# Kernel tuning notes

Measured on AMD Instinct MI355X. Metric: run time of the kernel, lower is better.

## Reference

```python
import jax, jax.numpy as jnp
import numpy as np

N_NODES = 100000
N_EDGES = 1600000
K = 48

def setup_inputs() -> dict:
    key = jax.random.key(0)
    ks = jax.random.split(key, 6)
    x = jax.random.normal(ks[0], (N_NODES, K), dtype=jnp.float32)
    pos_edge_index = jax.random.randint(ks[1], (2, N_EDGES), 0, N_NODES, dtype=jnp.int64)
    neg_edge_index = jax.random.randint(ks[2], (2, N_EDGES), 0, N_NODES, dtype=jnp.int64)
    # nn.Linear-style init (uniform +-1/sqrt(fan_in))
    lim1 = 1.0 / np.sqrt(3 * K)
    W1 = jax.random.uniform(ks[3], (3 * K, 16), minval=-lim1, maxval=lim1, dtype=jnp.float32)
    b1 = jnp.zeros((16,), dtype=jnp.float32)
    lim2 = 1.0 / np.sqrt(16)
    W2 = jax.random.uniform(ks[4], (16, K), minval=-lim2, maxval=lim2, dtype=jnp.float32)
    b2 = jnp.zeros((K,), dtype=jnp.float32)
    return {"x": x, "pos_edge_index": pos_edge_index, "neg_edge_index": neg_edge_index,
            "W1": W1, "b1": b1, "W2": W2, "b2": b2}

def _scatter_add_mp(x, edge_index):
    # PyG MessagePassing(aggr='add'), message = x_j:
    # gather source-node features and scatter-add into target nodes.
    src, dst = edge_index[0], edge_index[1]
    msgs = x[src]  # [E, k]
    return jax.ops.segment_sum(msgs, dst, num_segments=x.shape[0])  # [N, k]

def reference(x, pos_edge_index, neg_edge_index, W1, b1, W2, b2):
    x_pos = _scatter_add_mp(x, pos_edge_index)
    x_neg = _scatter_add_mp(x, neg_edge_index)
    out_cat = jnp.concatenate([x, x_pos, x_neg], axis=1)  # [N, 3k]
    h = jnp.tanh(out_cat @ W1 + b1)                        # [N, 16]
    C = h @ W2 + b2                                        # [N, k]
    return jax.nn.softmax(C, axis=1)
```

## Files before the change

### kernel.cpp

```cpp
#include <hip/hip_runtime.h>
#include <hip/hip_fp16.h>
#include <math.h>

#define NN 100000
#define NE 1600000
#define KF 48
#define NEDGE_ALL (2 * NE)

#define BKT_NODES 128
#define NBKT_PER  782
#define NBKT      1564
#define PACK_EPB  4096
#define NPB       782
#define OT2       1566
#define CAP2      2432
#define KSTG      10

typedef _Float16 half2v __attribute__((ext_vector_type(2)));
typedef _Float16 half4v __attribute__((ext_vector_type(4)));

#if defined(__has_builtin)
#if __has_builtin(__builtin_amdgcn_fdot2)
#define HAVE_FDOT2 1
#endif
#endif

__device__ __forceinline__ void acc_pair(float& ax, float& ay, half2v v)
{
#ifdef HAVE_FDOT2
    ax = __builtin_amdgcn_fdot2(v, (half2v){(_Float16)1.f, (_Float16)0.f}, ax, false);
    ay = __builtin_amdgcn_fdot2(v, (half2v){(_Float16)0.f, (_Float16)1.f}, ay, false);
#else
    ax += (float)v.x;
    ay += (float)v.y;
#endif
}

__global__ __launch_bounds__(512) void pack_kernel(
    const float* __restrict__ x,
    const int* __restrict__ ei_pos,
    const int* __restrict__ ei_neg,
    unsigned short* __restrict__ offT,
    unsigned* __restrict__ plist,
    __half* __restrict__ xh)
{
    {
        const float2* __restrict__ x2 = (const float2*)x;
        half2v* __restrict__ xhw = (half2v*)xh;
        const int n2 = (NN + 2) * (KF / 2);
        for (int i = blockIdx.x * 512 + threadIdx.x; i < n2; i += NPB * 512) {
            float2 v = (i < NN * (KF / 2)) ? x2[i] : make_float2(0.f, 0.f);
            xhw[i] = (half2v){(_Float16)v.x, (_Float16)v.y};
        }
    }

    __shared__ int cnt[NBKT];
    __shared__ int ps[391];
    __shared__ unsigned stage[PACK_EPB];

    const int t = threadIdx.x;
    for (int i = t; i < NBKT; i += 512) cnt[i] = 0;
    __syncthreads();

    unsigned pk[8];
    int bk[8];
    const int blockBase = blockIdx.x * PACK_EPB;
#pragma unroll
    for (int j = 0; j < 8; ++j) {
        int e = blockBase + j * 512 + t;
        bk[j] = -1;
        if (e < NEDGE_ALL) {
            int list = e >= NE;
            int ee = list ? e - NE : e;
            const int* ei = list ? ei_neg : ei_pos;
            int src = ei[ee];
            int dst = ei[NE + ee];
            int b = list * NBKT_PER + (dst >> 7);
            bk[j] = b;
            pk[j] = ((unsigned)(dst & 127) << 17) | (unsigned)src;
            atomicAdd(&cnt[b], 1);
        }
    }
    __syncthreads();

    int s0 = 0, s1 = 0, s2 = 0, s3 = 0;
    if (t < 391) {
        s0 = cnt[4 * t]; s1 = cnt[4 * t + 1]; s2 = cnt[4 * t + 2]; s3 = cnt[4 * t + 3];
        ps[t] = s0 + s1 + s2 + s3;
    }
    __syncthreads();
    for (int d = 1; d < 391; d <<= 1) {
        int v = (t < 391 && t >= d) ? ps[t - d] : 0;
        __syncthreads();
        if (t < 391) ps[t] += v;
        __syncthreads();
    }
    unsigned short* myrow = offT + (long)blockIdx.x * OT2;
    if (t < 391) {
        int base = t ? ps[t - 1] : 0;
        int o0 = base, o1 = o0 + s0, o2 = o1 + s1, o3 = o2 + s2;
        myrow[4 * t]     = (unsigned short)o0;
        myrow[4 * t + 1] = (unsigned short)o1;
        myrow[4 * t + 2] = (unsigned short)o2;
        myrow[4 * t + 3] = (unsigned short)o3;
        cnt[4 * t] = o0; cnt[4 * t + 1] = o1; cnt[4 * t + 2] = o2; cnt[4 * t + 3] = o3;
    }
    if (t == 390) myrow[NBKT] = (unsigned short)ps[390];
    __syncthreads();

#pragma unroll
    for (int j = 0; j < 8; ++j) {
        if (bk[j] >= 0) {
            int slot = atomicAdd(&cnt[bk[j]], 1);
            stage[slot] = pk[j];
        }
    }
    __syncthreads();

    {
        const uint4* __restrict__ st4 = (const uint4*)stage;
        uint4* __restrict__ out4 = (uint4*)(plist + (long)blockIdx.x * PACK_EPB);
#pragma unroll
        for (int j = 0; j < 2; ++j)
            out4[j * 512 + t] = st4[j * 512 + t];
    }
}

__global__ __launch_bounds__(256) void gather_kernel(
    const __half* __restrict__ xh,
    const unsigned* __restrict__ plist,
    const unsigned short* __restrict__ offT,
    float* __restrict__ xpos,
    float* __restrict__ xneg)
{
    __shared__ unsigned srt[CAP2];
    __shared__ int rb[NPB + 2];
    __shared__ unsigned short rsL[NPB];
    __shared__ int tmp[196];
    __shared__ int nh[BKT_NODES];
    __shared__ int starts[BKT_NODES];
    __shared__ int ends[BKT_NODES];
    __shared__ int cur2[BKT_NODES];

    const int b = blockIdx.x;
    const int t = threadIdx.x;

    for (int r = t; r < NPB; r += 256) {
        int s = offT[(long)r * OT2 + b];
        int e = offT[(long)r * OT2 + b + 1];
        rsL[r] = (unsigned short)s;
        srt[r] = (unsigned)(e - s);
    }
    if (t < BKT_NODES) nh[t] = 0;
    __syncthreads();

    int s0 = 0, s1 = 0, s2 = 0, s3 = 0;
    if (t < 196) {
        int i0 = 4 * t;
        s0 = (i0     < NPB) ? (int)srt[i0]     : 0;
        s1 = (i0 + 1 < NPB) ? (int)srt[i0 + 1] : 0;
        s2 = (i0 + 2 < NPB) ? (int)srt[i0 + 2] : 0;
        s3 = (i0 + 3 < NPB) ? (int)srt[i0 + 3] : 0;
        tmp[t] = s0 + s1 + s2 + s3;
    }
    __syncthreads();
    for (int d = 1; d < 196; d <<= 1) {
        int v = (t < 196 && t >= d) ? tmp[t - d] : 0;
        __syncthreads();
        if (t < 196) tmp[t] += v;
        __syncthreads();
    }
    if (t < 196) {
        int base = t ? tmp[t - 1] : 0;
        int i0 = 4 * t;
        if (i0     <= NPB) rb[i0]     = base;
        if (i0 + 1 <= NPB) rb[i0 + 1] = base + s0;
        if (i0 + 2 <= NPB) rb[i0 + 2] = base + s0 + s1;
        if (i0 + 3 <= NPB) rb[i0 + 3] = base + s0 + s1 + s2;
    }
    __syncthreads();
    int cb = rb[NPB];
    if (cb > CAP2) cb = CAP2;

    unsigned held[KSTG];
#pragma unroll
    for (int k = 0; k < KSTG; ++k) {
        int i = t + k * 256;
        held[k] = 0;
        if (i < cb) {
            int lo = 0, hi = NPB - 1;
#pragma unroll
            for (int it = 0; it < 10; ++it) {
                int mid = (lo + hi + 1) >> 1;
                bool ge = (rb[mid] <= i);
                lo = ge ? mid : lo;
                hi = ge ? hi : mid - 1;
            }
            unsigned p = plist[(long)lo * PACK_EPB + rsL[lo] + (i - rb[lo])];
            held[k] = p;
            atomicAdd(&nh[p >> 17], 1);
        }
    }
    __syncthreads();

    for (int d = 1; d < BKT_NODES; d <<= 1) {
        int v = 0;
        if (t < BKT_NODES && t >= d) v = nh[t - d];
        __syncthreads();
        if (t < BKT_NODES) nh[t] += v;
        __syncthreads();
    }
    if (t < BKT_NODES) {
        int e_ = min(nh[t], CAP2);
        int s_ = t ? min(nh[t - 1], CAP2) : 0;
        starts[t] = s_;
        ends[t] = e_;
        cur2[t] = s_;
    }
    __syncthreads();

#pragma unroll
    for (int k = 0; k < KSTG; ++k) {
        int i = t + k * 256;
        if (i < cb) {
            unsigned p = held[k];
            int slot = atomicAdd(&cur2[p >> 17], 1);
            if (slot < CAP2) srt[slot] = p;
        }
    }
    __syncthreads();

    const int wave = t >> 6, lane = t & 63;
    const int g = lane >> 4;
    const int sub = lane & 15;
    const int subc = (sub < 12) ? sub : 11;
    const int list = b >= NBKT_PER;
    const int nb = list ? b - NBKT_PER : b;
    float* o = list ? xneg : xpos;
    const half4v* __restrict__ xh4 = (const half4v*)xh;

    for (int n = wave; n < BKT_NODES; n += 4) {
        int gn = nb * BKT_NODES + n;
        if (gn >= NN) continue;
        int s = starts[n], e = ends[n];
        float a0 = 0.f, a1 = 0.f, a2 = 0.f, a3 = 0.f;
        for (int j = s; j < e; j += 16) {
            int i0 = j + g, i1 = j + 4 + g, i2 = j + 8 + g, i3 = j + 12 + g;
            int q0 = (i0 < e) ? (int)(srt[i0 < CAP2 ? i0 : 0] & 0x1FFFFu) : NN;
            int q1 = (i1 < e) ? (int)(srt[i1 < CAP2 ? i1 : 0] & 0x1FFFFu) : NN;
            int q2 = (i2 < e) ? (int)(srt[i2 < CAP2 ? i2 : 0] & 0x1FFFFu) : NN;
            int q3 = (i3 < e) ? (int)(srt[i3 < CAP2 ? i3 : 0] & 0x1FFFFu) : NN;
            half4v v0 = xh4[q0 * 12 + subc];
            half4v v1 = xh4[q1 * 12 + subc];
            half4v v2 = xh4[q2 * 12 + subc];
            half4v v3 = xh4[q3 * 12 + subc];
            acc_pair(a0, a1, (half2v){v0.x, v0.y});
            acc_pair(a2, a3, (half2v){v0.z, v0.w});
            acc_pair(a0, a1, (half2v){v1.x, v1.y});
            acc_pair(a2, a3, (half2v){v1.z, v1.w});
            acc_pair(a0, a1, (half2v){v2.x, v2.y});
            acc_pair(a2, a3, (half2v){v2.z, v2.w});
            acc_pair(a0, a1, (half2v){v3.x, v3.y});
            acc_pair(a2, a3, (half2v){v3.z, v3.w});
        }
        a0 += __shfl_xor(a0, 16); a0 += __shfl_xor(a0, 32);
        a1 += __shfl_xor(a1, 16); a1 += __shfl_xor(a1, 32);
        a2 += __shfl_xor(a2, 16); a2 += __shfl_xor(a2, 32);
        a3 += __shfl_xor(a3, 16); a3 += __shfl_xor(a3, 32);
        if (g == 0 && sub < 12) {
            float4* o4 = (float4*)o;
            o4[(long)gn * 12 + sub] = make_float4(a0, a1, a2, a3);
        }
    }
}

__global__ __launch_bounds__(256) void scatter2_kernel(
    const float* __restrict__ x,
    const int* __restrict__ ei_pos,
    const int* __restrict__ ei_neg,
    float* acc_pos,
    float* acc_neg)
{
    const int list = blockIdx.y;
    const int* ei = list ? ei_neg : ei_pos;
    float* acc = list ? acc_neg : acc_pos;

    long t = (long)blockIdx.x * blockDim.x + threadIdx.x;
    const long total = (long)NE * 12;
    if (t >= total) return;

    int e = (int)(t / 12);
    int r = (int)(t - (long)e * 12);
    int k4 = r * 4;

    int src = ei[e];
    int dst = ei[NE + e];

    const float4 v = *(const float4*)(x + (long)src * KF + k4);
    float* p = acc + (long)dst * KF + k4;

    unsafeAtomicAdd(p + 0, v.x);
    unsafeAtomicAdd(p + 1, v.y);
    unsafeAtomicAdd(p + 2, v.z);
    unsafeAtomicAdd(p + 3, v.w);
}

__global__ __launch_bounds__(256) void mlp_softmax_kernel(
    const float* __restrict__ x,
    const float* xpos,
    const float* __restrict__ xneg,
    const float* __restrict__ W1,
    const float* __restrict__ b1,
    const float* __restrict__ W2,
    const float* __restrict__ b2,
    float* out)
{
    __shared__ float sW1[144 * 16];
    __shared__ float sW2[16 * 48];
    __shared__ float sb1[16];
    __shared__ float sb2[48];

    for (int i = threadIdx.x; i < 144 * 16; i += blockDim.x) sW1[i] = W1[i];
    for (int i = threadIdx.x; i < 16 * 48;  i += blockDim.x) sW2[i] = W2[i];
    if (threadIdx.x < 16) sb1[threadIdx.x] = b1[threadIdx.x];
    if (threadIdx.x < 48) sb2[threadIdx.x] = b2[threadIdx.x];
    __syncthreads();

    const int n = blockIdx.x * blockDim.x + threadIdx.x;
    if (n >= NN) return;

    float h[16];
#pragma unroll
    for (int j = 0; j < 16; ++j) h[j] = sb1[j];

    const float* srcs[3];
    srcs[0] = x    + (long)n * KF;
    srcs[1] = xpos + (long)n * KF;
    srcs[2] = xneg + (long)n * KF;

    for (int s = 0; s < 3; ++s) {
        const float* px = srcs[s];
        for (int i = 0; i < KF; ++i) {
            const float v = px[i];
            const float* w = &sW1[(s * KF + i) * 16];
#pragma unroll
            for (int j = 0; j < 16; ++j) h[j] += v * w[j];
        }
    }
#pragma unroll
    for (int j = 0; j < 16; ++j) h[j] = tanhf(h[j]);

    float C[KF];
#pragma unroll
    for (int k = 0; k < KF; ++k) C[k] = sb2[k];
    for (int j = 0; j < 16; ++j) {
        const float hv = h[j];
        const float* w = &sW2[j * KF];
#pragma unroll
        for (int k = 0; k < KF; ++k) C[k] += hv * w[k];
    }

    float m = C[0];
#pragma unroll
    for (int k = 1; k < KF; ++k) m = fmaxf(m, C[k]);
    float ssum = 0.f;
#pragma unroll
    for (int k = 0; k < KF; ++k) { C[k] = expf(C[k] - m); ssum += C[k]; }
    const float inv = 1.0f / ssum;

    float* po = out + (long)n * KF;
#pragma unroll
    for (int k = 0; k < KF; ++k) po[k] = C[k] * inv;
}

extern "C" void kernel_launch(void* const* d_in, const int* in_sizes, int n_in,
                              void* d_out, int out_size, void* d_ws, size_t ws_size,
                              hipStream_t stream)
{
    const float* x      = (const float*)d_in[0];
    const int*   ei_pos = (const int*)  d_in[1];
    const int*   ei_neg = (const int*)  d_in[2];
    const float* W1     = (const float*)d_in[3];
    const float* b1     = (const float*)d_in[4];
    const float* W2     = (const float*)d_in[5];
    const float* b2     = (const float*)d_in[6];

    float* out  = (float*)d_out;
    float* xpos = (float*)d_out;

    const size_t acc_bytes   = (size_t)NN * KF * sizeof(float);
    const size_t plist_bytes = (size_t)NPB * PACK_EPB * sizeof(unsigned);
    const size_t offT_bytes  = (size_t)NPB * OT2 * sizeof(unsigned short);
    const size_t xh_bytes    = (size_t)(NN + 2) * KF * sizeof(__half);

    size_t off = 0;
    char* ws = (char*)d_ws;
    float*          xneg  = (float*)(ws + off);          off += acc_bytes;
    unsigned*       plist = (unsigned*)(ws + off);       off += plist_bytes;
    unsigned short* offT  = (unsigned short*)(ws + off); off += offT_bytes;
    __half*         xh    = (__half*)(ws + off);         off += xh_bytes;
    const size_t needed = off;

    if (ws_size >= needed) {
        pack_kernel<<<NPB, 512, 0, stream>>>(x, ei_pos, ei_neg, offT, plist, xh);
        gather_kernel<<<NBKT, 256, 0, stream>>>(xh, plist, offT, xpos, xneg);
    } else {
        hipMemsetAsync(xpos, 0, acc_bytes, stream);
        hipMemsetAsync(xneg, 0, acc_bytes, stream);
        const long total = (long)NE * 12;
        dim3 grid((unsigned)((total + 255) / 256), 2, 1);
        scatter2_kernel<<<grid, 256, 0, stream>>>(x, ei_pos, ei_neg, xpos, xneg);
    }

    mlp_softmax_kernel<<<(NN + 255) / 256, 256, 0, stream>>>(x, xpos, xneg, W1, b1, W2, b2, out);
}
```

Before: 234.3 us.

## Project features through W1 before gather to aggregate 16-wide instead of 48-wide

Uses linearity of the scatter-add and the first linear layer: each node's x is multiplied by the three W1 blocks up front in the pack kernel, so the gather aggregates 16-wide fp16 projections instead of 48-wide features. This cuts the random-gather bytes per edge by a factor of three and shrinks the intermediate buffers. A new MLP kernel adds the three partial pre-activations, applies tanh, the second layer and softmax. The costs are a per-node 144x16 matmul inside the pack kernel and rounding the projected values to fp16 before aggregation.

```diff
diff --git a/kernel.cpp b/kernel.cpp
--- a/kernel.cpp
+++ b/kernel.cpp
@@ -18,6 +18,7 @@
 
 typedef _Float16 half2v __attribute__((ext_vector_type(2)));
 typedef _Float16 half4v __attribute__((ext_vector_type(4)));
+typedef _Float16 half8v __attribute__((ext_vector_type(8)));
 
 #if defined(__has_builtin)
 #if __has_builtin(__builtin_amdgcn_fdot2)
@@ -40,27 +41,69 @@
     const float* __restrict__ x,
     const int* __restrict__ ei_pos,
     const int* __restrict__ ei_neg,
+    const float* __restrict__ W1,
+    const float* __restrict__ b1,
     unsigned short* __restrict__ offT,
     unsigned* __restrict__ plist,
-    __half* __restrict__ xh)
-{
-    {
-        const float2* __restrict__ x2 = (const float2*)x;
-        half2v* __restrict__ xhw = (half2v*)xh;
-        const int n2 = (NN + 2) * (KF / 2);
-        for (int i = blockIdx.x * 512 + threadIdx.x; i < n2; i += NPB * 512) {
-            float2 v = (i < NN * (KF / 2)) ? x2[i] : make_float2(0.f, 0.f);
-            xhw[i] = (half2v){(_Float16)v.x, (_Float16)v.y};
-        }
-    }
-
+    float* __restrict__ za,
+    __half* __restrict__ zbh,
+    __half* __restrict__ zch)
+{
     __shared__ int cnt[NBKT];
     __shared__ int ps[391];
     __shared__ unsigned stage[PACK_EPB];
+    __shared__ float sW1[144 * 16];
+    __shared__ float sb1[16];
 
     const int t = threadIdx.x;
+    for (int i = t; i < 144 * 16; i += 512) sW1[i] = W1[i];
+    if (t < 16) sb1[t] = b1[t];
     for (int i = t; i < NBKT; i += 512) cnt[i] = 0;
     __syncthreads();
+
+    {
+        const int n = blockIdx.x * 512 + t;
+        if (n < NN + 2) {
+            float aA[16], aB[16], aC[16];
+#pragma unroll
+            for (int j = 0; j < 16; ++j) { aA[j] = sb1[j]; aB[j] = 0.f; aC[j] = 0.f; }
+            if (n < NN) {
+                const float4* __restrict__ x4 = (const float4*)(x + (long)n * KF);
+                for (int i4 = 0; i4 < 12; ++i4) {
+                    float4 v = x4[i4];
+                    float vv[4] = {v.x, v.y, v.z, v.w};
+#pragma unroll
+                    for (int c = 0; c < 4; ++c) {
+                        const int f = i4 * 4 + c;
+                        const float* wA = &sW1[f * 16];
+                        const float* wB = &sW1[(48 + f) * 16];
+                        const float* wC = &sW1[(96 + f) * 16];
+                        const float s = vv[c];
+#pragma unroll
+                        for (int j = 0; j < 16; ++j) {
+                            aA[j] += s * wA[j];
+                            aB[j] += s * wB[j];
+                            aC[j] += s * wC[j];
+                        }
+                    }
+                }
+                float4* za4 = (float4*)(za + (long)n * 16);
+#pragma unroll
+                for (int j4 = 0; j4 < 4; ++j4)
+                    za4[j4] = make_float4(aA[4*j4], aA[4*j4+1], aA[4*j4+2], aA[4*j4+3]);
+            }
+            half8v hb0, hb1, hc0, hc1;
+#pragma unroll
+            for (int j = 0; j < 8; ++j) {
+                hb0[j] = (_Float16)aB[j];     hb1[j] = (_Float16)aB[8 + j];
+                hc0[j] = (_Float16)aC[j];     hc1[j] = (_Float16)aC[8 + j];
+            }
+            half8v* zb8 = (half8v*)zbh;
+            half8v* zc8 = (half8v*)zch;
+            zb8[(long)n * 2 + 0] = hb0;  zb8[(long)n * 2 + 1] = hb1;
+            zc8[(long)n * 2 + 0] = hc0;  zc8[(long)n * 2 + 1] = hc1;
+        }
+    }
 
     unsigned pk[8];
     int bk[8];
@@ -127,11 +170,12 @@
 }
 
 __global__ __launch_bounds__(256) void gather_kernel(
-    const __half* __restrict__ xh,
+    const __half* __restrict__ zbh,
+    const __half* __restrict__ zch,
     const unsigned* __restrict__ plist,
     const unsigned short* __restrict__ offT,
-    float* __restrict__ xpos,
-    float* __restrict__ xneg)
+    float* __restrict__ hpos,
+    float* __restrict__ hneg)
 {
     __shared__ unsigned srt[CAP2];
     __shared__ int rb[NPB + 2];
@@ -231,13 +275,12 @@
     __syncthreads();
 
     const int wave = t >> 6, lane = t & 63;
-    const int g = lane >> 4;
-    const int sub = lane & 15;
-    const int subc = (sub < 12) ? sub : 11;
+    const int g = lane >> 2;
+    const int sub = lane & 3;
     const int list = b >= NBKT_PER;
     const int nb = list ? b - NBKT_PER : b;
-    float* o = list ? xneg : xpos;
-    const half4v* __restrict__ xh4 = (const half4v*)xh;
+    float* o = list ? hneg : hpos;
+    const half4v* __restrict__ z4 = (const half4v*)(list ? zch : zbh);
 
     for (int n = wave; n < BKT_NODES; n += 4) {
         int gn = nb * BKT_NODES + n;
@@ -245,33 +288,75 @@
         int s = starts[n], e = ends[n];
         float a0 = 0.f, a1 = 0.f, a2 = 0.f, a3 = 0.f;
         for (int j = s; j < e; j += 16) {
-            int i0 = j + g, i1 = j + 4 + g, i2 = j + 8 + g, i3 = j + 12 + g;
-            int q0 = (i0 < e) ? (int)(srt[i0 < CAP2 ? i0 : 0] & 0x1FFFFu) : NN;
-            int q1 = (i1 < e) ? (int)(srt[i1 < CAP2 ? i1 : 0] & 0x1FFFFu) : NN;
-            int q2 = (i2 < e) ? (int)(srt[i2 < CAP2 ? i2 : 0] & 0x1FFFFu) : NN;
-            int q3 = (i3 < e) ? (int)(srt[i3 < CAP2 ? i3 : 0] & 0x1FFFFu) : NN;
-            half4v v0 = xh4[q0 * 12 + subc];
-            half4v v1 = xh4[q1 * 12 + subc];
-            half4v v2 = xh4[q2 * 12 + subc];
-            half4v v3 = xh4[q3 * 12 + subc];
-            acc_pair(a0, a1, (half2v){v0.x, v0.y});
-            acc_pair(a2, a3, (half2v){v0.z, v0.w});
-            acc_pair(a0, a1, (half2v){v1.x, v1.y});
-            acc_pair(a2, a3, (half2v){v1.z, v1.w});
-            acc_pair(a0, a1, (half2v){v2.x, v2.y});
-            acc_pair(a2, a3, (half2v){v2.z, v2.w});
-            acc_pair(a0, a1, (half2v){v3.x, v3.y});
-            acc_pair(a2, a3, (half2v){v3.z, v3.w});
-        }
-        a0 += __shfl_xor(a0, 16); a0 += __shfl_xor(a0, 32);
-        a1 += __shfl_xor(a1, 16); a1 += __shfl_xor(a1, 32);
-        a2 += __shfl_xor(a2, 16); a2 += __shfl_xor(a2, 32);
-        a3 += __shfl_xor(a3, 16); a3 += __shfl_xor(a3, 32);
-        if (g == 0 && sub < 12) {
+            int i0 = j + g;
+            int q = (i0 < e) ? (int)(srt[i0 < CAP2 ? i0 : 0] & 0x1FFFFu) : NN;
+            half4v v = z4[q * 4 + sub];
+            acc_pair(a0, a1, (half2v){v.x, v.y});
+            acc_pair(a2, a3, (half2v){v.z, v.w});
+        }
+        a0 += __shfl_xor(a0, 4); a0 += __shfl_xor(a0, 8); a0 += __shfl_xor(a0, 16); a0 += __shfl_xor(a0, 32);
+        a1 += __shfl_xor(a1, 4); a1 += __shfl_xor(a1, 8); a1 += __shfl_xor(a1, 16); a1 += __shfl_xor(a1, 32);
+        a2 += __shfl_xor(a2, 4); a2 += __shfl_xor(a2, 8); a2 += __shfl_xor(a2, 16); a2 += __shfl_xor(a2, 32);
+        a3 += __shfl_xor(a3, 4); a3 += __shfl_xor(a3, 8); a3 += __shfl_xor(a3, 16); a3 += __shfl_xor(a3, 32);
+        if (g == 0) {
             float4* o4 = (float4*)o;
-            o4[(long)gn * 12 + sub] = make_float4(a0, a1, a2, a3);
-        }
-    }
+            o4[(long)gn * 4 + sub] = make_float4(a0, a1, a2, a3);
+        }
+    }
+}
+
+__global__ __launch_bounds__(256) void mlp2_kernel(
+    const float* __restrict__ za,
+    const float* __restrict__ hpos,
+    const float* __restrict__ hneg,
+    const float* __restrict__ W2,
+    const float* __restrict__ b2,
+    float* __restrict__ out)
+{
+    __shared__ float sW2[16 * 48];
+    __shared__ float sb2[48];
+    for (int i = threadIdx.x; i < 16 * 48; i += 256) sW2[i] = W2[i];
+    if (threadIdx.x < 48) sb2[threadIdx.x] = b2[threadIdx.x];
+    __syncthreads();
+
+    const int n = blockIdx.x * 256 + threadIdx.x;
+    if (n >= NN) return;
+
+    const float4* A = (const float4*)(za   + (long)n * 16);
+    const float4* P = (const float4*)(hpos + (long)n * 16);
+    const float4* Q = (const float4*)(hneg + (long)n * 16);
+    float h[16];
+#pragma unroll
+    for (int j4 = 0; j4 < 4; ++j4) {
+        float4 a = A[j4], p = P[j4], q = Q[j4];
+        h[4 * j4 + 0] = tanhf(a.x + p.x + q.x);
+        h[4 * j4 + 1] = tanhf(a.y + p.y + q.y);
+        h[4 * j4 + 2] = tanhf(a.z + p.z + q.z);
+        h[4 * j4 + 3] = tanhf(a.w + p.w + q.w);
+    }
+
+    float C[KF];
+#pragma unroll
+    for (int k = 0; k < KF; ++k) C[k] = sb2[k];
+    for (int j = 0; j < 16; ++j) {
+        const float hv = h[j];
+        const float* w = &sW2[j * KF];
+#pragma unroll
+        for (int k = 0; k < KF; ++k) C[k] += hv * w[k];
+    }
+
+    float m = C[0];
+#pragma unroll
+    for (int k = 1; k < KF; ++k) m = fmaxf(m, C[k]);
+    float ssum = 0.f;
+#pragma unroll
+    for (int k = 0; k < KF; ++k) { C[k] = expf(C[k] - m); ssum += C[k]; }
+    const float inv = 1.0f / ssum;
+
+    float4* po = (float4*)(out + (long)n * KF);
+#pragma unroll
+    for (int k4 = 0; k4 < 12; ++k4)
+        po[k4] = make_float4(C[4*k4] * inv, C[4*k4+1] * inv, C[4*k4+2] * inv, C[4*k4+3] * inv);
 }
 
 __global__ __launch_bounds__(256) void scatter2_kernel(
@@ -385,32 +470,38 @@
     const float* W2     = (const float*)d_in[5];
     const float* b2     = (const float*)d_in[6];
 
-    float* out  = (float*)d_out;
-    float* xpos = (float*)d_out;
-
-    const size_t acc_bytes   = (size_t)NN * KF * sizeof(float);
+    float* out = (float*)d_out;
+
+    const size_t h_bytes     = (size_t)NN * 16 * sizeof(float);
+    const size_t za_bytes    = (size_t)NN * 16 * sizeof(float);
+    const size_t zh_bytes    = (size_t)(NN + 2) * 16 * sizeof(__half);
     const size_t plist_bytes = (size_t)NPB * PACK_EPB * sizeof(unsigned);
     const size_t offT_bytes  = (size_t)NPB * OT2 * sizeof(unsigned short);
-    const size_t xh_bytes    = (size_t)(NN + 2) * KF * sizeof(__half);
 
     size_t off = 0;
     char* ws = (char*)d_ws;
-    float*          xneg  = (float*)(ws + off);          off += acc_bytes;
+    float*          hpos  = (float*)(ws + off);          off += h_bytes;
+    float*          hneg  = (float*)(ws + off);          off += h_bytes;
+    float*          za    = (float*)(ws + off);          off += za_bytes;
+    __half*         zbh   = (__half*)(ws + off);         off += zh_bytes;
+    __half*         zch   = (__half*)(ws + off);         off += zh_bytes;
     unsigned*       plist = (unsigned*)(ws + off);       off += plist_bytes;
     unsigned short* offT  = (unsigned short*)(ws + off); off += offT_bytes;
-    __half*         xh    = (__half*)(ws + off);         off += xh_bytes;
     const size_t needed = off;
 
     if (ws_size >= needed) {
-        pack_kernel<<<NPB, 512, 0, stream>>>(x, ei_pos, ei_neg, offT, plist, xh);
-        gather_kernel<<<NBKT, 256, 0, stream>>>(xh, plist, offT, xpos, xneg);
+        pack_kernel<<<NPB, 512, 0, stream>>>(x, ei_pos, ei_neg, W1, b1, offT, plist, za, zbh, zch);
+        gather_kernel<<<NBKT, 256, 0, stream>>>(zbh, zch, plist, offT, hpos, hneg);
+        mlp2_kernel<<<(NN + 255) / 256, 256, 0, stream>>>(za, hpos, hneg, W2, b2, out);
     } else {
+        float* xpos = (float*)d_out;
+        float* xneg = (float*)d_ws;
+        const size_t acc_bytes = (size_t)NN * KF * sizeof(float);
         hipMemsetAsync(xpos, 0, acc_bytes, stream);
         hipMemsetAsync(xneg, 0, acc_bytes, stream);
         const long total = (long)NE * 12;
         dim3 grid((unsigned)((total + 255) / 256), 2, 1);
         scatter2_kernel<<<grid, 256, 0, stream>>>(x, ei_pos, ei_neg, xpos, xneg);
-    }
-
-    mlp_softmax_kernel<<<(NN + 255) / 256, 256, 0, stream>>>(x, xpos, xneg, W1, b1, W2, b2, out);
-}
+        mlp_softmax_kernel<<<(NN + 255) / 256, 256, 0, stream>>>(x, xpos, xneg, W1, b1, W2, b2, out);
+    }
+}
```

Result: faster. 204.2 us (-12.9%).
